# Kernel optimization log

Measured on AMD Instinct MI355X. Metric: run time of the kernel, lower is better.

The kernel has to match this reference:

```python
import jax, jax.numpy as jnp
import numpy as np


def setup_inputs() -> dict:
    key = jax.random.key(0)
    k1, k2, k3, k4, k5, k6 = jax.random.split(key, 6)
    N, M = 4096, 4096      # data matrix
    K, D = 2048, 1024      # parameter matrix K x K, similarity matrix K x D
    Npair = 128            # size of i/j index subsets
    return {
        "actual": jax.random.normal(k1, (N, M), dtype=jnp.float32),
        "prediction": jax.random.normal(k2, (N, M), dtype=jnp.float32),
        "lamb": jnp.asarray(0.1, dtype=jnp.float32),
        "P": jax.random.normal(k3, (K, K), dtype=jnp.float32),
        "S": jax.random.normal(k4, (K, D), dtype=jnp.float32),
        "i_indices": jax.random.randint(k5, (Npair,), 0, K, dtype=jnp.int64),
        "j_indices": jax.random.randint(k6, (Npair,), 0, K, dtype=jnp.int64),
    }


def _safe_norm_rows(diff):
    # L2 norm over last axis with a zero-safe sqrt (grad is 0 at exactly-0 diffs,
    # matching torch's subgradient convention for .norm()).
    d2 = jnp.sum(diff * diff, axis=-1)
    pos = d2 > 0
    return jnp.sqrt(jnp.where(pos, d2, 1.0)) * pos


def reference(actual, prediction, lamb, P, S, i_indices, j_indices):
    # (p > 0) * clamp(p, min=0) == relu(p)
    Pp = jnp.maximum(P, 0.0)
    # penalty term: ||relu(P)||_F
    penalty = jnp.linalg.norm(Pp)
    # pairwise parameter-similarity penalty:
    # sum_{i in I, j in J} relu(P)[i,j] * || S[i,:] - S[j,:] ||_2
    Si = S[i_indices]                       # [Ni, D]
    Sj = S[j_indices]                       # [Nj, D]
    diff = Si[:, None, :] - Sj[None, :, :]  # [Ni, Nj, D]
    norms = _safe_norm_rows(diff)           # [Ni, Nj]
    Pij = Pp[i_indices[:, None], j_indices[None, :]]  # [Ni, Nj]
    parameter_penalty = jnp.sum(Pij * norms)
    data_term = jnp.linalg.norm(actual - prediction)
    return data_term + lamb * (penalty + parameter_penalty)
```

## Files before the change

kernel.cpp:

```cpp
#include <hip/hip_runtime.h>
#include <math.h>

#define BP  1024
#define BR  1024
#define TPB 256

__device__ __forceinline__ float waveReduceSum(float v) {
    #pragma unroll
    for (int off = 32; off > 0; off >>= 1)
        v += __shfl_down(v, off, 64);
    return v;
}

#define CONS(AV, PV, S) { float d_;                       \
    d_ = (AV).x - (PV).x; S += d_ * d_;                   \
    d_ = (AV).y - (PV).y; S += d_ * d_;                   \
    d_ = (AV).z - (PV).z; S += d_ * d_;                   \
    d_ = (AV).w - (PV).w; S += d_ * d_; }

#define RCONS(V, S) { float r_;                           \
    r_ = fmaxf((V).x, 0.f); S += r_ * r_;                 \
    r_ = fmaxf((V).y, 0.f); S += r_ * r_;                 \
    r_ = fmaxf((V).z, 0.f); S += r_ * r_;                 \
    r_ = fmaxf((V).w, 0.f); S += r_ * r_; }

__global__ __launch_bounds__(TPB, 8)
void fused_kernel(const float* __restrict__ a,
                  const float* __restrict__ p,
                  const float* __restrict__ Pm,
                  const float* __restrict__ S,
                  const int* __restrict__ ii,
                  const int* __restrict__ jj,
                  float* __restrict__ ws,
                  long nAP, long nP, int Npair, int D, int K)
{
    __shared__ float sm0[4], sm1[4];
    const int wave = threadIdx.x >> 6;
    const int lane = threadIdx.x & 63;
    const int bid  = blockIdx.x;

    if (bid < BP) {
        const int totalPairs = Npair * Npair;
        const int base = bid * 16 + wave * 4;
        float local = 0.f;

        if (base < totalPairs && D == 1024 && (base % Npair) + 3 < Npair) {
            const int ig = base / Npair;
            const int j0 = base - ig * Npair;
            const int ri = ii[ig];
            const float4* Si4 = (const float4*)(S + (long)ri * D);
            float4 x0 = Si4[lane];
            float4 x1 = Si4[lane + 64];
            float4 x2 = Si4[lane + 128];
            float4 x3 = Si4[lane + 192];
            const long riK = (long)ri * K;

            float d2q[4];
            int   rjq[4];
            #pragma unroll
            for (int q = 0; q < 4; ++q) {
                const int rj = jj[j0 + q];
                rjq[q] = rj;
                const float4* Sj4 = (const float4*)(S + (long)rj * D);
                float4 y0 = Sj4[lane];
                float4 y1 = Sj4[lane + 64];
                float4 y2 = Sj4[lane + 128];
                float4 y3 = Sj4[lane + 192];
                float d2 = 0.f, e;
                e = x0.x - y0.x; d2 += e * e;
                e = x0.y - y0.y; d2 += e * e;
                e = x0.z - y0.z; d2 += e * e;
                e = x0.w - y0.w; d2 += e * e;
                e = x1.x - y1.x; d2 += e * e;
                e = x1.y - y1.y; d2 += e * e;
                e = x1.z - y1.z; d2 += e * e;
                e = x1.w - y1.w; d2 += e * e;
                e = x2.x - y2.x; d2 += e * e;
                e = x2.y - y2.y; d2 += e * e;
                e = x2.z - y2.z; d2 += e * e;
                e = x2.w - y2.w; d2 += e * e;
                e = x3.x - y3.x; d2 += e * e;
                e = x3.y - y3.y; d2 += e * e;
                e = x3.z - y3.z; d2 += e * e;
                e = x3.w - y3.w; d2 += e * e;
                d2q[q] = d2;
            }
            #pragma unroll
            for (int q = 0; q < 4; ++q)
                d2q[q] = waveReduceSum(d2q[q]);
            if (lane == 0) {
                #pragma unroll
                for (int q = 0; q < 4; ++q)
                    if (d2q[q] > 0.f)
                        local += fmaxf(Pm[riK + rjq[q]], 0.f) * sqrtf(d2q[q]);
            }
        } else {
            #pragma unroll
            for (int q = 0; q < 4; ++q) {
                int pair = base + q;
                if (pair < totalPairs) {
                    int ig = pair / Npair;
                    int j  = pair - ig * Npair;
                    int ri = ii[ig];
                    int rj = jj[j];
                    const float* Si = S + (long)ri * D;
                    const float* Sj = S + (long)rj * D;
                    float d2 = 0.f;
                    for (int c = lane; c < D; c += 64) {
                        float e = Si[c] - Sj[c];
                        d2 += e * e;
                    }
                    d2 = waveReduceSum(d2);
                    if (lane == 0 && d2 > 0.f)
                        local += fmaxf(Pm[(long)ri * K + rj], 0.f) * sqrtf(d2);
                }
            }
        }
        if (lane == 0) sm0[wave] = local;
        __syncthreads();
        if (threadIdx.x == 0)
            ws[2 * BR + bid] = sm0[0] + sm0[1] + sm0[2] + sm0[3];
    } else {
        const int  rb     = bid - BP;
        const long tid    = (long)rb * TPB + threadIdx.x;
        const long stride = (long)BR * TPB;

        const float4* a4 = (const float4*)a;
        const float4* p4 = (const float4*)p;
        const long n4  = nAP >> 2;
        const long nP4 = nP  >> 2;

        float s0a = 0.f, s0b = 0.f, s0c = 0.f, s0d = 0.f;

        if (n4 == 16L * stride) {
            float4 A[2][4], Pv[2][4];
            long i = tid;
            #pragma unroll
            for (int u = 0; u < 4; ++u) {
                A[0][u]  = a4[i + u * stride];
                Pv[0][u] = p4[i + u * stride];
            }
            i += 4 * stride;
            #pragma unroll
            for (int it = 1; it < 4; ++it) {
                const int nxt = it & 1;
                const int cur = nxt ^ 1;
                #pragma unroll
                for (int u = 0; u < 4; ++u) {
                    A[nxt][u]  = a4[i + u * stride];
                    Pv[nxt][u] = p4[i + u * stride];
                }
                i += 4 * stride;
                __builtin_amdgcn_sched_barrier(0);
                CONS(A[cur][0], Pv[cur][0], s0a);
                CONS(A[cur][1], Pv[cur][1], s0b);
                CONS(A[cur][2], Pv[cur][2], s0c);
                CONS(A[cur][3], Pv[cur][3], s0d);
            }
            CONS(A[1][0], Pv[1][0], s0a);
            CONS(A[1][1], Pv[1][1], s0b);
            CONS(A[1][2], Pv[1][2], s0c);
            CONS(A[1][3], Pv[1][3], s0d);
        } else {
            for (long i = tid; i < n4; i += stride) {
                float4 av = a4[i], pv = p4[i];
                CONS(av, pv, s0a);
            }
        }

        const float4* P4 = (const float4*)Pm;
        float s1a = 0.f, s1b = 0.f;
        if (nP4 == 4L * stride) {
            float4 B0 = P4[tid];
            float4 B1 = P4[tid + stride];
            float4 B2 = P4[tid + 2 * stride];
            float4 B3 = P4[tid + 3 * stride];
            __builtin_amdgcn_sched_barrier(0);
            RCONS(B0, s1a); RCONS(B1, s1b);
            RCONS(B2, s1a); RCONS(B3, s1b);
        } else {
            for (long q = tid; q < nP4; q += stride) {
                float4 v = P4[q];
                RCONS(v, s1a);
            }
        }

        float s0 = waveReduceSum(s0a + s0b + s0c + s0d);
        float s1 = waveReduceSum(s1a + s1b);
        if (lane == 0) { sm0[wave] = s0; sm1[wave] = s1; }
        __syncthreads();
        if (threadIdx.x == 0) {
            ws[rb]      = sm0[0] + sm0[1] + sm0[2] + sm0[3];
            ws[BR + rb] = sm1[0] + sm1[1] + sm1[2] + sm1[3];
        }
    }
}

__global__ void finalize_kernel(const float* __restrict__ ws,
                                const float* __restrict__ lamb,
                                float* __restrict__ out)
{
    float a0 = 0.f, a1 = 0.f, a2 = 0.f;
    for (int i = threadIdx.x; i < BR; i += TPB) {
        a0 += ws[i];
        a1 += ws[BR + i];
    }
    for (int i = threadIdx.x; i < BP; i += TPB)
        a2 += ws[2 * BR + i];

    a0 = waveReduceSum(a0);
    a1 = waveReduceSum(a1);
    a2 = waveReduceSum(a2);

    __shared__ float m0[4], m1[4], m2[4];
    int wave = threadIdx.x >> 6;
    int lane = threadIdx.x & 63;
    if (lane == 0) { m0[wave] = a0; m1[wave] = a1; m2[wave] = a2; }
    __syncthreads();
    if (threadIdx.x == 0) {
        float A0 = m0[0] + m0[1] + m0[2] + m0[3];
        float A1 = m1[0] + m1[1] + m1[2] + m1[3];
        float A2 = m2[0] + m2[1] + m2[2] + m2[3];
        out[0] = sqrtf(A0) + lamb[0] * (sqrtf(A1) + A2);
    }
}

extern "C" void kernel_launch(void* const* d_in, const int* in_sizes, int n_in,
                              void* d_out, int out_size, void* d_ws, size_t ws_size,
                              hipStream_t stream) {
    const float* actual = (const float*)d_in[0];
    const float* pred   = (const float*)d_in[1];
    const float* lamb   = (const float*)d_in[2];
    const float* Pm     = (const float*)d_in[3];
    const float* S      = (const float*)d_in[4];
    const int*   ii     = (const int*)d_in[5];
    const int*   jj     = (const int*)d_in[6];
    float* out = (float*)d_out;
    float* ws  = (float*)d_ws;

    long nAP   = in_sizes[0];
    long nP    = in_sizes[3];
    int  K     = (int)lround(sqrt((double)nP));
    int  Npair = in_sizes[5];
    int  D     = (int)(in_sizes[4] / K);

    fused_kernel<<<BP + BR, TPB, 0, stream>>>(actual, pred, Pm, S, ii, jj, ws,
                                              nAP, nP, Npair, D, K);
    finalize_kernel<<<1, TPB, 0, stream>>>(ws, lamb, out);
}
```

Baseline: 35.42 us.

## Merge pair-norm and streaming reduction roles into one block type

Each block now does both the streaming reduction over actual/prediction and P and a slice of the pairwise S-row distances, instead of splitting blocks into two specialised groups. This halves the grid to 1024 blocks, keeps every block doing the bandwidth-heavy stream, and lets the pair work overlap within the same wave's timeline. The launch-bounds occupancy hint is lowered from 8 to 4 blocks per CU, and finalize now reads partials as float4. The risk is more register pressure and serialising the pair work after the stream within each block, instead of running it in separate concurrent blocks.

```diff
diff --git a/kernel.cpp b/kernel.cpp
--- a/kernel.cpp
+++ b/kernel.cpp
@@ -1,8 +1,7 @@
 #include <hip/hip_runtime.h>
 #include <math.h>
 
-#define BP  1024
-#define BR  1024
+#define NB  1024
 #define TPB 256
 
 __device__ __forceinline__ float waveReduceSum(float v) {
@@ -24,7 +23,7 @@
     r_ = fmaxf((V).z, 0.f); S += r_ * r_;                 \
     r_ = fmaxf((V).w, 0.f); S += r_ * r_; }
 
-__global__ __launch_bounds__(TPB, 8)
+__global__ __launch_bounds__(TPB, 4)
 void fused_kernel(const float* __restrict__ a,
                   const float* __restrict__ p,
                   const float* __restrict__ Pm,
@@ -34,165 +33,156 @@
                   float* __restrict__ ws,
                   long nAP, long nP, int Npair, int D, int K)
 {
-    __shared__ float sm0[4], sm1[4];
+    __shared__ float sm0[4], sm1[4], sm2[4];
     const int wave = threadIdx.x >> 6;
     const int lane = threadIdx.x & 63;
     const int bid  = blockIdx.x;
 
-    if (bid < BP) {
-        const int totalPairs = Npair * Npair;
-        const int base = bid * 16 + wave * 4;
-        float local = 0.f;
-
-        if (base < totalPairs && D == 1024 && (base % Npair) + 3 < Npair) {
-            const int ig = base / Npair;
-            const int j0 = base - ig * Npair;
-            const int ri = ii[ig];
-            const float4* Si4 = (const float4*)(S + (long)ri * D);
-            float4 x0 = Si4[lane];
-            float4 x1 = Si4[lane + 64];
-            float4 x2 = Si4[lane + 128];
-            float4 x3 = Si4[lane + 192];
-            const long riK = (long)ri * K;
-
-            float d2q[4];
-            int   rjq[4];
+    const long tid    = (long)bid * TPB + threadIdx.x;
+    const long stride = (long)NB * TPB;
+
+    const float4* a4 = (const float4*)a;
+    const float4* p4 = (const float4*)p;
+    const long n4  = nAP >> 2;
+    const long nP4 = nP  >> 2;
+
+    float s0a = 0.f, s0b = 0.f, s0c = 0.f, s0d = 0.f;
+
+    if (n4 == 16L * stride) {
+        float4 A[2][4], Pv[2][4];
+        long i = tid;
+        #pragma unroll
+        for (int u = 0; u < 4; ++u) {
+            A[0][u]  = a4[i + u * stride];
+            Pv[0][u] = p4[i + u * stride];
+        }
+        i += 4 * stride;
+        #pragma unroll
+        for (int it = 1; it < 4; ++it) {
+            const int nxt = it & 1;
+            const int cur = nxt ^ 1;
             #pragma unroll
-            for (int q = 0; q < 4; ++q) {
-                const int rj = jj[j0 + q];
-                rjq[q] = rj;
-                const float4* Sj4 = (const float4*)(S + (long)rj * D);
-                float4 y0 = Sj4[lane];
-                float4 y1 = Sj4[lane + 64];
-                float4 y2 = Sj4[lane + 128];
-                float4 y3 = Sj4[lane + 192];
-                float d2 = 0.f, e;
-                e = x0.x - y0.x; d2 += e * e;
-                e = x0.y - y0.y; d2 += e * e;
-                e = x0.z - y0.z; d2 += e * e;
-                e = x0.w - y0.w; d2 += e * e;
-                e = x1.x - y1.x; d2 += e * e;
-                e = x1.y - y1.y; d2 += e * e;
-                e = x1.z - y1.z; d2 += e * e;
-                e = x1.w - y1.w; d2 += e * e;
-                e = x2.x - y2.x; d2 += e * e;
-                e = x2.y - y2.y; d2 += e * e;
-                e = x2.z - y2.z; d2 += e * e;
-                e = x2.w - y2.w; d2 += e * e;
-                e = x3.x - y3.x; d2 += e * e;
-                e = x3.y - y3.y; d2 += e * e;
-                e = x3.z - y3.z; d2 += e * e;
-                e = x3.w - y3.w; d2 += e * e;
-                d2q[q] = d2;
+            for (int u = 0; u < 4; ++u) {
+                A[nxt][u]  = a4[i + u * stride];
+                Pv[nxt][u] = p4[i + u * stride];
             }
+            i += 4 * stride;
+            __builtin_amdgcn_sched_barrier(0);
+            CONS(A[cur][0], Pv[cur][0], s0a);
+            CONS(A[cur][1], Pv[cur][1], s0b);
+            CONS(A[cur][2], Pv[cur][2], s0c);
+            CONS(A[cur][3], Pv[cur][3], s0d);
+        }
+        CONS(A[1][0], Pv[1][0], s0a);
+        CONS(A[1][1], Pv[1][1], s0b);
+        CONS(A[1][2], Pv[1][2], s0c);
+        CONS(A[1][3], Pv[1][3], s0d);
+    } else {
+        for (long i = tid; i < n4; i += stride) {
+            float4 av = a4[i], pv = p4[i];
+            CONS(av, pv, s0a);
+        }
+    }
+
+    const float4* P4 = (const float4*)Pm;
+    float s1a = 0.f, s1b = 0.f;
+    if (nP4 == 4L * stride) {
+        float4 B0 = P4[tid];
+        float4 B1 = P4[tid + stride];
+        float4 B2 = P4[tid + 2 * stride];
+        float4 B3 = P4[tid + 3 * stride];
+        __builtin_amdgcn_sched_barrier(0);
+        RCONS(B0, s1a); RCONS(B1, s1b);
+        RCONS(B2, s1a); RCONS(B3, s1b);
+    } else {
+        for (long q = tid; q < nP4; q += stride) {
+            float4 v = P4[q];
+            RCONS(v, s1a);
+        }
+    }
+
+    float s0 = waveReduceSum(s0a + s0b + s0c + s0d);
+    float s1 = waveReduceSum(s1a + s1b);
+    if (lane == 0) { sm0[wave] = s0; sm1[wave] = s1; }
+
+    const long totalPairs = (long)Npair * Npair;
+    const long base = ((long)bid * 4 + wave) * 4;
+    float local = 0.f;
+
+    if (D == 1024 && base + 3 < totalPairs && (base % Npair) + 3 < Npair) {
+        const int ig = (int)(base / Npair);
+        const int j0 = (int)(base - (long)ig * Npair);
+        const int ri = ii[ig];
+        const float4* Si4 = (const float4*)(S + (long)ri * D);
+        float4 x0 = Si4[lane];
+        float4 x1 = Si4[lane + 64];
+        float4 x2 = Si4[lane + 128];
+        float4 x3 = Si4[lane + 192];
+        const long riK = (long)ri * K;
+
+        float d2q[4];
+        int   rjq[4];
+        #pragma unroll
+        for (int q = 0; q < 4; ++q) {
+            const int rj = jj[j0 + q];
+            rjq[q] = rj;
+            const float4* Sj4 = (const float4*)(S + (long)rj * D);
+            float4 y0 = Sj4[lane];
+            float4 y1 = Sj4[lane + 64];
+            float4 y2 = Sj4[lane + 128];
+            float4 y3 = Sj4[lane + 192];
+            float d2 = 0.f, e;
+            e = x0.x - y0.x; d2 += e * e;
+            e = x0.y - y0.y; d2 += e * e;
+            e = x0.z - y0.z; d2 += e * e;
+            e = x0.w - y0.w; d2 += e * e;
+            e = x1.x - y1.x; d2 += e * e;
+            e = x1.y - y1.y; d2 += e * e;
+            e = x1.z - y1.z; d2 += e * e;
+            e = x1.w - y1.w; d2 += e * e;
+            e = x2.x - y2.x; d2 += e * e;
+            e = x2.y - y2.y; d2 += e * e;
+            e = x2.z - y2.z; d2 += e * e;
+            e = x2.w - y2.w; d2 += e * e;
+            e = x3.x - y3.x; d2 += e * e;
+            e = x3.y - y3.y; d2 += e * e;
+            e = x3.z - y3.z; d2 += e * e;
+            e = x3.w - y3.w; d2 += e * e;
+            d2q[q] = d2;
+        }
+        #pragma unroll
+        for (int q = 0; q < 4; ++q)
+            d2q[q] = waveReduceSum(d2q[q]);
+        if (lane == 0) {
             #pragma unroll
             for (int q = 0; q < 4; ++q)
-                d2q[q] = waveReduceSum(d2q[q]);
-            if (lane == 0) {
-                #pragma unroll
-                for (int q = 0; q < 4; ++q)
-                    if (d2q[q] > 0.f)
-                        local += fmaxf(Pm[riK + rjq[q]], 0.f) * sqrtf(d2q[q]);
+                if (d2q[q] > 0.f)
+                    local += fmaxf(Pm[riK + rjq[q]], 0.f) * sqrtf(d2q[q]);
+        }
+    } else {
+        for (long pr = base; pr < base + 4 && pr < totalPairs; ++pr) {
+            int ig = (int)(pr / Npair);
+            int j  = (int)(pr - (long)ig * Npair);
+            int ri = ii[ig];
+            int rj = jj[j];
+            const float* Si = S + (long)ri * D;
+            const float* Sj = S + (long)rj * D;
+            float d2 = 0.f;
+            for (int c = lane; c < D; c += 64) {
+                float e = Si[c] - Sj[c];
+                d2 += e * e;
             }
-        } else {
-            #pragma unroll
-            for (int q = 0; q < 4; ++q) {
-                int pair = base + q;
-                if (pair < totalPairs) {
-                    int ig = pair / Npair;
-                    int j  = pair - ig * Npair;
-                    int ri = ii[ig];
-                    int rj = jj[j];
-                    const float* Si = S + (long)ri * D;
-                    const float* Sj = S + (long)rj * D;
-                    float d2 = 0.f;
-                    for (int c = lane; c < D; c += 64) {
-                        float e = Si[c] - Sj[c];
-                        d2 += e * e;
-                    }
-                    d2 = waveReduceSum(d2);
-                    if (lane == 0 && d2 > 0.f)
-                        local += fmaxf(Pm[(long)ri * K + rj], 0.f) * sqrtf(d2);
-                }
-            }
-        }
-        if (lane == 0) sm0[wave] = local;
-        __syncthreads();
-        if (threadIdx.x == 0)
-            ws[2 * BR + bid] = sm0[0] + sm0[1] + sm0[2] + sm0[3];
-    } else {
-        const int  rb     = bid - BP;
-        const long tid    = (long)rb * TPB + threadIdx.x;
-        const long stride = (long)BR * TPB;
-
-        const float4* a4 = (const float4*)a;
-        const float4* p4 = (const float4*)p;
-        const long n4  = nAP >> 2;
-        const long nP4 = nP  >> 2;
-
-        float s0a = 0.f, s0b = 0.f, s0c = 0.f, s0d = 0.f;
-
-        if (n4 == 16L * stride) {
-            float4 A[2][4], Pv[2][4];
-            long i = tid;
-            #pragma unroll
-            for (int u = 0; u < 4; ++u) {
-                A[0][u]  = a4[i + u * stride];
-                Pv[0][u] = p4[i + u * stride];
-            }
-            i += 4 * stride;
-            #pragma unroll
-            for (int it = 1; it < 4; ++it) {
-                const int nxt = it & 1;
-                const int cur = nxt ^ 1;
-                #pragma unroll
-                for (int u = 0; u < 4; ++u) {
-                    A[nxt][u]  = a4[i + u * stride];
-                    Pv[nxt][u] = p4[i + u * stride];
-                }
-                i += 4 * stride;
-                __builtin_amdgcn_sched_barrier(0);
-                CONS(A[cur][0], Pv[cur][0], s0a);
-                CONS(A[cur][1], Pv[cur][1], s0b);
-                CONS(A[cur][2], Pv[cur][2], s0c);
-                CONS(A[cur][3], Pv[cur][3], s0d);
-            }
-            CONS(A[1][0], Pv[1][0], s0a);
-            CONS(A[1][1], Pv[1][1], s0b);
-            CONS(A[1][2], Pv[1][2], s0c);
-            CONS(A[1][3], Pv[1][3], s0d);
-        } else {
-            for (long i = tid; i < n4; i += stride) {
-                float4 av = a4[i], pv = p4[i];
-                CONS(av, pv, s0a);
-            }
-        }
-
-        const float4* P4 = (const float4*)Pm;
-        float s1a = 0.f, s1b = 0.f;
-        if (nP4 == 4L * stride) {
-            float4 B0 = P4[tid];
-            float4 B1 = P4[tid + stride];
-            float4 B2 = P4[tid + 2 * stride];
-            float4 B3 = P4[tid + 3 * stride];
-            __builtin_amdgcn_sched_barrier(0);
-            RCONS(B0, s1a); RCONS(B1, s1b);
-            RCONS(B2, s1a); RCONS(B3, s1b);
-        } else {
-            for (long q = tid; q < nP4; q += stride) {
-                float4 v = P4[q];
-                RCONS(v, s1a);
-            }
-        }
-
-        float s0 = waveReduceSum(s0a + s0b + s0c + s0d);
-        float s1 = waveReduceSum(s1a + s1b);
-        if (lane == 0) { sm0[wave] = s0; sm1[wave] = s1; }
-        __syncthreads();
-        if (threadIdx.x == 0) {
-            ws[rb]      = sm0[0] + sm0[1] + sm0[2] + sm0[3];
-            ws[BR + rb] = sm1[0] + sm1[1] + sm1[2] + sm1[3];
-        }
+            d2 = waveReduceSum(d2);
+            if (lane == 0 && d2 > 0.f)
+                local += fmaxf(Pm[(long)ri * K + rj], 0.f) * sqrtf(d2);
+        }
+    }
+    if (lane == 0) sm2[wave] = local;
+    __syncthreads();
+    if (threadIdx.x == 0) {
+        ws[bid]          = sm0[0] + sm0[1] + sm0[2] + sm0[3];
+        ws[NB + bid]     = sm1[0] + sm1[1] + sm1[2] + sm1[3];
+        ws[2 * NB + bid] = sm2[0] + sm2[1] + sm2[2] + sm2[3];
     }
 }
 
@@ -201,12 +191,15 @@
                                 float* __restrict__ out)
 {
     float a0 = 0.f, a1 = 0.f, a2 = 0.f;
-    for (int i = threadIdx.x; i < BR; i += TPB) {
-        a0 += ws[i];
-        a1 += ws[BR + i];
-    }
-    for (int i = threadIdx.x; i < BP; i += TPB)
-        a2 += ws[2 * BR + i];
+    const float4* w4 = (const float4*)ws;
+    for (int i = threadIdx.x; i < NB / 4; i += TPB) {
+        float4 v = w4[i];
+        a0 += v.x + v.y + v.z + v.w;
+        float4 u = w4[NB / 4 + i];
+        a1 += u.x + u.y + u.z + u.w;
+        float4 t = w4[2 * (NB / 4) + i];
+        a2 += t.x + t.y + t.z + t.w;
+    }
 
     a0 = waveReduceSum(a0);
     a1 = waveReduceSum(a1);
@@ -244,7 +237,7 @@
     int  Npair = in_sizes[5];
     int  D     = (int)(in_sizes[4] / K);
 
-    fused_kernel<<<BP + BR, TPB, 0, stream>>>(actual, pred, Pm, S, ii, jj, ws,
-                                              nAP, nP, Npair, D, K);
+    fused_kernel<<<NB, TPB, 0, stream>>>(actual, pred, Pm, S, ii, jj, ws,
+                                         nAP, nP, Npair, D, K);
     finalize_kernel<<<1, TPB, 0, stream>>>(ws, lamb, out);
 }
```

New measurement: 37.97 us. +7.2%, slower.
